# Performance work log

Hardware: AMD Instinct MI355X
Metric: run time of the kernel (lower is better)

## Reference

```python
import jax, jax.numpy as jnp
import numpy as np

N_TOK, TOKDIM = 2048, 1024
NHEADS, KDIM = 16, 64


def setup_inputs() -> dict:
    key = jax.random.key(0)
    kg, kk, kq = jax.random.split(key, 3)
    g = jax.random.normal(kg, (N_TOK, TOKDIM), dtype=jnp.float32)
    # params use normal(stddev=0.002) init, as in the flax module
    Wk = 0.002 * jax.random.normal(kk, (NHEADS, KDIM, TOKDIM), dtype=jnp.float32)
    Wq = 0.002 * jax.random.normal(kq, (NHEADS, KDIM, TOKDIM), dtype=jnp.float32)
    return {"g": g, "Wk": Wk, "Wq": Wq}


def reference(g, Wk, Wq):
    """manual_grad of the attention energy: returns d(energy)/dg, shape [n, d]."""
    H, Z, D = Wk.shape
    betas = jnp.full((H,), 1.0, dtype=g.dtype) / jnp.sqrt(jnp.asarray(Z, g.dtype))
    K = jnp.einsum('hzd,kd->khz', Wk, g)   # [n,h,z]
    Q = jnp.einsum('hzd,qd->qhz', Wq, g)   # [n,h,z]
    F1 = jnp.einsum('hzd,khz->khd', Wq, K)  # [n,h,d]
    F2 = jnp.einsum('hzd,qhz->qhd', Wk, Q)  # [n,h,d]
    A1 = jnp.einsum('h,khz,qhz->hqk', betas, K, Q)  # [h,q,k] scores
    A2 = jax.nn.softmax(A1, -1)
    T1 = -jnp.einsum('khd,hqk->qd', F1, A2)
    T2 = -jnp.einsum('qhd,hqk->kd', F2, A2)
    return T1 + T2
```

## Files before the change

### kernel.cpp

```cpp
#include <hip/hip_runtime.h>
#include <stdint.h>

#define NT 2048
#define TD 1024
#define NH 16
static constexpr float SCL = 0.18033688011112042f;

typedef __attribute__((ext_vector_type(8))) short bf16x8;
typedef __attribute__((ext_vector_type(4))) float f32x4;
typedef __attribute__((ext_vector_type(16))) float f32x16;
typedef __attribute__((address_space(3))) uint32_t lds_u32;
typedef __attribute__((address_space(1))) uint32_t glb_u32;

__device__ __forceinline__ float bf2f(unsigned short u){
  union { uint32_t u32; float f; } v; v.u32 = ((uint32_t)u) << 16; return v.f;
}
__device__ __forceinline__ unsigned short f2bf(float f){
  union { float f; uint32_t u; } v; v.f = f;
  uint32_t r = v.u + 0x7fffu + ((v.u >> 16) & 1u);
  return (unsigned short)(r >> 16);
}
__device__ __forceinline__ bf16x8 ld8(const unsigned short* base, int row, int kc){
  return *(const bf16x8*)((const char*)base + row*128 + ((kc ^ (row & 7)) << 4));
}
template<int N> __device__ __forceinline__ void wait_vm_lgkm0(){
  if constexpr (N == 0)      asm volatile("s_waitcnt vmcnt(0) lgkmcnt(0)" ::: "memory");
  else if constexpr (N == 4) asm volatile("s_waitcnt vmcnt(4) lgkmcnt(0)" ::: "memory");
  else if constexpr (N == 6) asm volatile("s_waitcnt vmcnt(6) lgkmcnt(0)" ::: "memory");
  __builtin_amdgcn_sched_barrier(0);
}

__global__ __launch_bounds__(256) void prep_kernel(
    const float* __restrict__ g, const float* __restrict__ Wk, const float* __restrict__ Wq,
    unsigned short* __restrict__ gbf, unsigned short* __restrict__ wkq,
    unsigned short* __restrict__ TWP)
{
  int b = blockIdx.x;
  if (b < 1024) {
    int base = b * 2048 + threadIdx.x;
    #pragma unroll
    for (int i = 0; i < 8; i++) { int idx = base + i * 256; gbf[idx] = f2bf(g[idx]); }
  } else if (b < 2048) {
    int base = (b - 1024) * 2048 + threadIdx.x;
    #pragma unroll
    for (int i = 0; i < 8; i++) {
      int idx = base + i * 256;
      float v = (idx < (1 << 20)) ? Wk[idx] : Wq[idx - (1 << 20)];
      wkq[idx] = f2bf(v);
    }
  } else {
    int t = b - 2048;
    int db = t & 31, jzg = t >> 5;
    int d0 = db * 32, j0 = jzg * 128;
    __shared__ unsigned short tile[128][33];
    int tid = threadIdx.x;
    const float* src = (j0 < 1024) ? Wq : Wk;
    int jb = (j0 < 1024) ? j0 : (j0 - 1024);
    #pragma unroll
    for (int i = 0; i < 16; i++) {
      int idx = i * 256 + tid, r = idx >> 5, c = idx & 31;
      tile[r][c] = f2bf(src[(size_t)(jb + r) * 1024 + d0 + c]);
    }
    __syncthreads();
    int jq = tid >> 6, l = tid & 63;
    #pragma unroll
    for (int f = 0; f < 2; f++) {
      int jzl = jq * 2 + f;
      unsigned short ob[8];
      #pragma unroll
      for (int e = 0; e < 8; e++)
        ob[e] = tile[jzl * 16 + 8 * (l >> 5) + e][l & 31];
      unsigned short* dst = TWP + ((size_t)(db * 128 + jzg * 8 + jzl) * 64 + l) * 8;
      *(ushort4*)dst       = *(ushort4*)&ob[0];
      *(ushort4*)(dst + 4) = *(ushort4*)&ob[4];
    }
  }
}

__global__ __launch_bounds__(256) void pack_pck(const unsigned short* __restrict__ CKQ,
                                                unsigned short* __restrict__ PCK)
{
  int tile = blockIdx.x;
  int cb = tile >> 6, rb = tile & 63;
  __shared__ unsigned short t[32][72];
  int tid = threadIdx.x;
  int r = tid >> 3, c0 = (tid & 7) * 8;
  const unsigned short* src = CKQ + (size_t)(rb * 32 + r) * 2048 + cb * 64 + c0;
  *(ushort4*)&t[r][c0]     = *(const ushort4*)src;
  *(ushort4*)&t[r][c0 + 4] = *(const ushort4*)(src + 4);
  __syncthreads();
  int kz = tid >> 6, l = tid & 63;
  int zl = kz * 16 + 8 * (l >> 5);
  ushort4 lo = *(ushort4*)&t[l & 31][zl];
  ushort4 hi4 = *(ushort4*)&t[l & 31][zl + 4];
  unsigned short* dst = PCK + ((size_t)(tile * 4 + kz) * 64 + l) * 8;
  *(ushort4*)dst       = lo;
  *(ushort4*)(dst + 4) = hi4;
}

template<bool DIVL>
__global__ __launch_bounds__(256) void pack_pbx(const unsigned short* __restrict__ CKQ,
                                                const float* __restrict__ L,
                                                unsigned short* __restrict__ PBX)
{
  int bid = blockIdx.x;
  int qb = bid & 63, hz = bid >> 6;
  int h = hz >> 1, zb = hz & 1;
  int colbase = (DIVL ? 1024 : 0) + h * 64 + zb * 32;
  __shared__ unsigned short tq[32][36];
  __shared__ float rcpL[32];
  int tid = threadIdx.x;
  int r = tid >> 3, c0 = (tid & 7) * 4;
  *(ushort4*)&tq[r][c0] =
      *(const ushort4*)(CKQ + (size_t)(qb * 32 + r) * 2048 + colbase + c0);
  if (DIVL && tid < 32) rcpL[tid] = 1.0f / L[(size_t)h * NT + qb * 32 + tid];
  __syncthreads();
  if (tid < 128) {
    int ks = tid >> 6, l = tid & 63;
    int zl = l & 31, hi = l >> 5;
    unsigned short ob[8];
    #pragma unroll
    for (int e = 0; e < 8; e++) {
      int ql = 16 * ks + 8 * (e >> 2) + 4 * hi + (e & 3);
      unsigned short v = tq[ql][zl];
      if (DIVL) v = f2bf(bf2f(v) * rcpL[ql]);
      ob[e] = v;
    }
    unsigned short* dst = PBX + ((size_t)(bid * 2 + ks) * 64 + l) * 8;
    *(ushort4*)dst       = *(ushort4*)&ob[0];
    *(ushort4*)(dst + 4) = *(ushort4*)&ob[4];
  }
}

template<int TM, int TN, int EPI, int WPE>
__global__ __launch_bounds__(256, WPE) void btg2_kernel(
    const unsigned short* __restrict__ A, int lda,
    const unsigned short* __restrict__ BT, int ldb,
    int Kdim, void* C0)
{
  constexpr int WM = TM / 2, WN = TN / 2, FM = WM / 16, FN = WN / 16;
  constexpr int AC = TM / 32, BC = TN / 32, LOADS = AC + BC;
  __shared__ __align__(16) unsigned short As[3][TM * 64];
  __shared__ __align__(16) unsigned short Bs[3][TN * 64];
  int tid = threadIdx.x, lane = tid & 63, wave = tid >> 6;
  int wr = wave >> 1, wc = wave & 1, lrow = lane & 15, g = lane >> 4;
  int bm = blockIdx.x * TM, bn = blockIdx.y * TN;

  auto stage = [&](unsigned short* bufA, unsigned short* bufB, int kk) {
    #pragma unroll
    for (int i = 0; i < AC; i++) {
      int c = i * 256 + tid, row = c >> 3, sl = ((c & 7) ^ (row & 7)) << 3;
      __builtin_amdgcn_global_load_lds((glb_u32*)(A + (size_t)(bm + row) * lda + kk + sl),
          (lds_u32*)((char*)bufA + i * 4096 + wave * 1024), 16, 0, 0);
    }
    #pragma unroll
    for (int i = 0; i < BC; i++) {
      int c = i * 256 + tid, row = c >> 3, sl = ((c & 7) ^ (row & 7)) << 3;
      __builtin_amdgcn_global_load_lds((glb_u32*)(BT + (size_t)(bn + row) * ldb + kk + sl),
          (lds_u32*)((char*)bufB + i * 4096 + wave * 1024), 16, 0, 0);
    }
  };

  f32x4 acc[FM][FN] = {};
  int nt = Kdim >> 6;
  stage(As[0], Bs[0], 0);
  stage(As[1], Bs[1], 64);
  wait_vm_lgkm0<LOADS>();
  __builtin_amdgcn_s_barrier();
  int bc = 0;
  for (int t = 0; t < nt; t++) {
    int bp = bc + 2; if (bp >= 3) bp -= 3;
    if (t + 2 < nt) stage(As[bp], Bs[bp], (t + 2) * 64);
    const unsigned short* Ac = As[bc];
    const unsigned short* Bc = Bs[bc];
    #pragma unroll
    for (int k2 = 0; k2 < 2; k2++) {
      bf16x8 a_[FM], b_[FN];
      #pragma unroll
      for (int m = 0; m < FM; m++) a_[m] = ld8(Ac, wr * WM + m * 16 + lrow, k2 * 4 + g);
      #pragma unroll
      for (int n = 0; n < FN; n++) b_[n] = ld8(Bc, wc * WN + n * 16 + lrow, k2 * 4 + g);
      #pragma unroll
      for (int m = 0; m < FM; m++)
        #pragma unroll
        for (int n = 0; n < FN; n++)
          acc[m][n] = __builtin_amdgcn_mfma_f32_16x16x32_bf16(a_[m], b_[n], acc[m][n], 0, 0, 0);
    }
    if (t + 2 < nt) wait_vm_lgkm0<LOADS>(); else wait_vm_lgkm0<0>();
    __builtin_amdgcn_s_barrier();
    bc = (bc == 2) ? 0 : bc + 1;
  }
  #pragma unroll
  for (int m = 0; m < FM; m++) {
    int rb = bm + wr * WM + m * 16 + 4 * g;
    #pragma unroll
    for (int n = 0; n < FN; n++) {
      int cc = bn + wc * WN + n * 16 + lrow;
      f32x4 v = acc[m][n];
      unsigned short* Cp = (unsigned short*)C0;
      #pragma unroll
      for (int j = 0; j < 4; j++) Cp[(size_t)(rb + j) * 2048 + cc] = f2bf(v[j]);
    }
  }
}

template<bool DIV>
__global__ __launch_bounds__(256, 2) void fused_kernel(
    const unsigned short* __restrict__ PCK,
    const unsigned short* __restrict__ PBX,
    unsigned short* __restrict__ PA,
    float* __restrict__ Lg)
{
  __shared__ __align__(16) float Red[2][64][68];
  __shared__ float L_lds[64];
  int tid = threadIdx.x, l = tid & 63, w = tid >> 6;
  int zr = l & 31, hi = l >> 5;
  int lin = blockIdx.x;
  int wgid = (lin & 7) * 64 + (lin >> 3);
  int h = wgid >> 5, pB = wgid & 31, p0 = pB * 64;
  int cbA = DIV ? h : 16 + h;
  int cbB = DIV ? 16 + h : h;
  const bf16x8* PCKf = (const bf16x8*)PCK;
  const bf16x8* PBXf = (const bf16x8*)PBX;

  bf16x8 bs[2][4];
  #pragma unroll
  for (int ps = 0; ps < 2; ps++)
    #pragma unroll
    for (int kz = 0; kz < 4; kz++)
      bs[ps][kz] = PCKf[((size_t)(cbB * 64 + pB * 2 + ps) * 4 + kz) * 64 + l];

  auto load = [&](bf16x8 (&a_)[4], bf16x8 (&pb_)[2][2], int rb){
    #pragma unroll
    for (int kz = 0; kz < 4; kz++)
      a_[kz] = PCKf[((size_t)(cbA * 64 + rb) * 4 + kz) * 64 + l];
    #pragma unroll
    for (int zb = 0; zb < 2; zb++)
      #pragma unroll
      for (int ks = 0; ks < 2; ks++)
        pb_[zb][ks] = PBXf[((size_t)((h * 2 + zb) * 64 + rb) * 2 + ks) * 64 + l];
  };

  f32x16 acc_pv[2][2] = {};
  float lsum[2] = {0.f, 0.f};
  bf16x8 a_c[4], pb_c[2][2];
  load(a_c, pb_c, w * 16);

  for (int t = 0; t < 16; t++) {
    bf16x8 a_n[4], pb_n[2][2];
    if (t + 1 < 16) load(a_n, pb_n, w * 16 + t + 1);
    f32x16 acc_s[2] = {};
    #pragma unroll
    for (int kz = 0; kz < 4; kz++) {
      acc_s[0] = __builtin_amdgcn_mfma_f32_32x32x16_bf16(a_c[kz], bs[0][kz], acc_s[0], 0, 0, 0);
      acc_s[1] = __builtin_amdgcn_mfma_f32_32x32x16_bf16(a_c[kz], bs[1][kz], acc_s[1], 0, 0, 0);
    }
    union { bf16x8 v; uint32_t u[4]; } pu[2][2];
    #pragma unroll
    for (int ps = 0; ps < 2; ps++) {
      float ev[16];
      #pragma unroll
      for (int r = 0; r < 16; r++) ev[r] = exp2f(acc_s[ps][r] * SCL);
      if (DIV) {
        #pragma unroll
        for (int r = 0; r < 16; r++) lsum[ps] += ev[r];
      }
      #pragma unroll
      for (int ks = 0; ks < 2; ks++)
        #pragma unroll
        for (int i = 0; i < 4; i++)
          asm("v_cvt_pk_bf16_f32 %0, %1, %2"
              : "=v"(pu[ps][ks].u[i]) : "v"(ev[8 * ks + 2 * i]), "v"(ev[8 * ks + 2 * i + 1]));
    }
    #pragma unroll
    for (int zb = 0; zb < 2; zb++)
      #pragma unroll
      for (int ks = 0; ks < 2; ks++) {
        acc_pv[0][zb] = __builtin_amdgcn_mfma_f32_32x32x16_bf16(pu[0][ks].v, pb_c[zb][ks], acc_pv[0][zb], 0, 0, 0);
        acc_pv[1][zb] = __builtin_amdgcn_mfma_f32_32x32x16_bf16(pu[1][ks].v, pb_c[zb][ks], acc_pv[1][zb], 0, 0, 0);
      }
    #pragma unroll
    for (int kz = 0; kz < 4; kz++) a_c[kz] = a_n[kz];
    #pragma unroll
    for (int zb = 0; zb < 2; zb++)
      #pragma unroll
      for (int ks = 0; ks < 2; ks++) pb_c[zb][ks] = pb_n[zb][ks];
  }

  if (w >= 2) {
    #pragma unroll
    for (int ps = 0; ps < 2; ps++)
      #pragma unroll
      for (int zb = 0; zb < 2; zb++) {
        int z = zb * 32 + zr;
        #pragma unroll
        for (int u = 0; u < 4; u++) {
          int p = ps * 32 + 8 * u + 4 * hi;
          f32x4 q;
          q[0] = acc_pv[ps][zb][4 * u];     q[1] = acc_pv[ps][zb][4 * u + 1];
          q[2] = acc_pv[ps][zb][4 * u + 2]; q[3] = acc_pv[ps][zb][4 * u + 3];
          *(f32x4*)&Red[w - 2][z][p] = q;
        }
      }
  }
  if (DIV && tid < 64) L_lds[tid] = 0.f;
  __syncthreads();
  if (w < 2) {
    #pragma unroll
    for (int ps = 0; ps < 2; ps++)
      #pragma unroll
      for (int zb = 0; zb < 2; zb++) {
        int z = zb * 32 + zr;
        #pragma unroll
        for (int u = 0; u < 4; u++) {
          int p = ps * 32 + 8 * u + 4 * hi;
          float* slot = &Red[w][z][p];
          f32x4 q = *(f32x4*)slot;
          q[0] += acc_pv[ps][zb][4 * u];     q[1] += acc_pv[ps][zb][4 * u + 1];
          q[2] += acc_pv[ps][zb][4 * u + 2]; q[3] += acc_pv[ps][zb][4 * u + 3];
          *(f32x4*)slot = q;
        }
      }
  }
  if (DIV) {
    #pragma unroll
    for (int ps = 0; ps < 2; ps++) {
      float s = lsum[ps];
      s += __shfl_xor(s, 32);
      if (hi == 0) atomicAdd(&L_lds[ps * 32 + zr], s);
    }
  }
  __syncthreads();
  if (DIV && tid < 64) Lg[(size_t)h * NT + p0 + tid] = L_lds[tid];
  int p = tid >> 2, z16 = (tid & 3) * 16;
  float inv = DIV ? 1.0f / L_lds[p] : 1.0f;
  int cbase = DIV ? h * 64 : TD + h * 64;
  int jz = (cbase + z16) >> 4;
  int tok = p0 + p, tb = tok >> 5, tl = tok & 31;
  unsigned short ob[16];
  #pragma unroll
  for (int i = 0; i < 16; i++) {
    int z = z16 + i;
    float x = Red[0][z][p] + Red[1][z][p];
    ob[i] = f2bf(x * inv);
  }
  unsigned short* dst = PA + (((size_t)jz * 64 + tb) * 64) * 8;
  *(ushort4*)(dst + tl * 8)            = *(ushort4*)&ob[0];
  *(ushort4*)(dst + tl * 8 + 4)        = *(ushort4*)&ob[4];
  *(ushort4*)(dst + (32 + tl) * 8)     = *(ushort4*)&ob[8];
  *(ushort4*)(dst + (32 + tl) * 8 + 4) = *(ushort4*)&ob[12];
}

__global__ __launch_bounds__(256, 2) void out_kernel(
    const unsigned short* __restrict__ PA,
    const unsigned short* __restrict__ TWP,
    float* __restrict__ out)
{
  __shared__ __align__(16) float Red[2][64][68];
  int tid = threadIdx.x, l = tid & 63, w = tid >> 6;
  int zr = l & 31, hi = l >> 5;
  int lin = blockIdx.x;
  int wgid = (lin & 7) * 64 + (lin >> 3);
  int tokb = wgid >> 4, db2 = wgid & 15;
  const bf16x8* PAf = (const bf16x8*)PA;
  const bf16x8* TWf = (const bf16x8*)TWP;

  f32x16 acc[2][2] = {};
  bf16x8 a_c[2], b_c[2];
  auto loadx = [&](bf16x8 (&a_)[2], bf16x8 (&b_)[2], int jz){
    #pragma unroll
    for (int th = 0; th < 2; th++)
      a_[th] = PAf[((size_t)jz * 64 + tokb * 2 + th) * 64 + l];
    #pragma unroll
    for (int dh = 0; dh < 2; dh++)
      b_[dh] = TWf[((size_t)(db2 * 2 + dh) * 128 + jz) * 64 + l];
  };
  loadx(a_c, b_c, w * 32);
  for (int it = 0; it < 32; it++) {
    bf16x8 a_n[2], b_n[2];
    if (it + 1 < 32) loadx(a_n, b_n, w * 32 + it + 1);
    #pragma unroll
    for (int th = 0; th < 2; th++)
      #pragma unroll
      for (int dh = 0; dh < 2; dh++)
        acc[th][dh] = __builtin_amdgcn_mfma_f32_32x32x16_bf16(a_c[th], b_c[dh], acc[th][dh], 0, 0, 0);
    #pragma unroll
    for (int i = 0; i < 2; i++) { a_c[i] = a_n[i]; b_c[i] = b_n[i]; }
  }
  if (w >= 2) {
    #pragma unroll
    for (int th = 0; th < 2; th++)
      #pragma unroll
      for (int dh = 0; dh < 2; dh++) {
        int d = dh * 32 + zr;
        #pragma unroll
        for (int u = 0; u < 4; u++) {
          int tk = th * 32 + 8 * u + 4 * hi;
          f32x4 q;
          q[0] = acc[th][dh][4 * u];     q[1] = acc[th][dh][4 * u + 1];
          q[2] = acc[th][dh][4 * u + 2]; q[3] = acc[th][dh][4 * u + 3];
          *(f32x4*)&Red[w - 2][d][tk] = q;
        }
      }
  }
  __syncthreads();
  if (w < 2) {
    #pragma unroll
    for (int th = 0; th < 2; th++)
      #pragma unroll
      for (int dh = 0; dh < 2; dh++) {
        int d = dh * 32 + zr;
        #pragma unroll
        for (int u = 0; u < 4; u++) {
          int tk = th * 32 + 8 * u + 4 * hi;
          float* slot = &Red[w][d][tk];
          f32x4 q = *(f32x4*)slot;
          q[0] += acc[th][dh][4 * u];     q[1] += acc[th][dh][4 * u + 1];
          q[2] += acc[th][dh][4 * u + 2]; q[3] += acc[th][dh][4 * u + 3];
          *(f32x4*)slot = q;
        }
      }
  }
  __syncthreads();
  int p = tid >> 2, d16 = (tid & 3) * 16;
  float* dst = out + (size_t)(tokb * 64 + p) * 1024 + db2 * 64 + d16;
  #pragma unroll
  for (int i4 = 0; i4 < 16; i4 += 4) {
    f32x4 r;
    #pragma unroll
    for (int j = 0; j < 4; j++)
      r[j] = -(Red[0][d16 + i4 + j][p] + Red[1][d16 + i4 + j][p]);
    *(f32x4*)(dst + i4) = r;
  }
}

extern "C" void kernel_launch(void* const* d_in, const int* in_sizes, int n_in,
                              void* d_out, int out_size, void* d_ws, size_t ws_size,
                              hipStream_t stream)
{
  (void)in_sizes; (void)n_in; (void)out_size; (void)ws_size;
  const float* g  = (const float*)d_in[0];
  const float* Wk = (const float*)d_in[1];
  const float* Wq = (const float*)d_in[2];

  char* ws = (char*)d_ws;
  size_t off = 0;
  auto alloc = [&](size_t b) -> char* {
    char* p = ws + off; off += (b + 255) & ~((size_t)255); return p;
  };
  unsigned short* gbf  = (unsigned short*)alloc((size_t)NT * TD * 2);
  unsigned short* wkq  = (unsigned short*)alloc((size_t)2 * TD * TD * 2);
  unsigned short* TWP  = (unsigned short*)alloc((size_t)TD * 2048 * 2);
  unsigned short* CKQ  = (unsigned short*)alloc((size_t)NT * 2048 * 2);
  unsigned short* PCK  = (unsigned short*)alloc((size_t)NT * 2048 * 2);
  unsigned short* PBT  = (unsigned short*)alloc((size_t)TD * NT * 2);
  unsigned short* QSTP = (unsigned short*)alloc((size_t)TD * NT * 2);
  unsigned short* PA   = (unsigned short*)alloc((size_t)NT * 2048 * 2);
  float*          Lbuf = (float*)alloc((size_t)NH * NT * 4);

  prep_kernel<<<dim3(2560), dim3(256), 0, stream>>>(g, Wk, Wq, gbf, wkq, TWP);

  btg2_kernel<128, 64, 0, 2><<<dim3(16, 32), dim3(256), 0, stream>>>(
      gbf, TD, wkq, TD, TD, (void*)CKQ);

  pack_pck<<<dim3(2048), dim3(256), 0, stream>>>(CKQ, PCK);
  pack_pbx<false><<<dim3(2048), dim3(256), 0, stream>>>(CKQ, nullptr, PBT);

  fused_kernel<true><<<dim3(512), dim3(256), 0, stream>>>(PCK, PBT, PA, Lbuf);

  pack_pbx<true><<<dim3(2048), dim3(256), 0, stream>>>(CKQ, Lbuf, QSTP);

  fused_kernel<false><<<dim3(512), dim3(256), 0, stream>>>(PCK, QSTP, PA, nullptr);

  out_kernel<<<dim3(512), dim3(256), 0, stream>>>(PA, TWP, (float*)d_out);
}
```

Measured before the change: 107.1 us.

## Pre-pack operands into MFMA fragment layout and fuse K/Q projection with PCK packing

The prep kernel now writes g and the Wk/Wq weights directly in a per-lane MFMA fragment layout. A new kq_kernel computes the K/Q projection with 32x32x16 MFMAs, using register double-buffered loads straight from global memory and an LDS reduction across the split-K waves. It writes both the row-major CKQ and the packed PCK layout, so the separate pack_pck launch and its CKQ reread are gone. In exchange it drops the LDS-staged, swizzled, triple-buffered GEMM and relies on fragment-coalesced global loads plus a split-K reduction through shared memory.

```diff
diff --git a/kernel.cpp b/kernel.cpp
--- a/kernel.cpp
+++ b/kernel.cpp
@@ -9,8 +9,6 @@
 typedef __attribute__((ext_vector_type(8))) short bf16x8;
 typedef __attribute__((ext_vector_type(4))) float f32x4;
 typedef __attribute__((ext_vector_type(16))) float f32x16;
-typedef __attribute__((address_space(3))) uint32_t lds_u32;
-typedef __attribute__((address_space(1))) uint32_t glb_u32;
 
 __device__ __forceinline__ float bf2f(unsigned short u){
   union { uint32_t u32; float f; } v; v.u32 = ((uint32_t)u) << 16; return v.f;
@@ -20,40 +18,43 @@
   uint32_t r = v.u + 0x7fffu + ((v.u >> 16) & 1u);
   return (unsigned short)(r >> 16);
 }
-__device__ __forceinline__ bf16x8 ld8(const unsigned short* base, int row, int kc){
-  return *(const bf16x8*)((const char*)base + row*128 + ((kc ^ (row & 7)) << 4));
-}
-template<int N> __device__ __forceinline__ void wait_vm_lgkm0(){
-  if constexpr (N == 0)      asm volatile("s_waitcnt vmcnt(0) lgkmcnt(0)" ::: "memory");
-  else if constexpr (N == 4) asm volatile("s_waitcnt vmcnt(4) lgkmcnt(0)" ::: "memory");
-  else if constexpr (N == 6) asm volatile("s_waitcnt vmcnt(6) lgkmcnt(0)" ::: "memory");
-  __builtin_amdgcn_sched_barrier(0);
-}
 
 __global__ __launch_bounds__(256) void prep_kernel(
     const float* __restrict__ g, const float* __restrict__ Wk, const float* __restrict__ Wq,
-    unsigned short* __restrict__ gbf, unsigned short* __restrict__ wkq,
+    unsigned short* __restrict__ PG, unsigned short* __restrict__ PW,
     unsigned short* __restrict__ TWP)
 {
   int b = blockIdx.x;
-  if (b < 1024) {
-    int base = b * 2048 + threadIdx.x;
-    #pragma unroll
-    for (int i = 0; i < 8; i++) { int idx = base + i * 256; gbf[idx] = f2bf(g[idx]); }
-  } else if (b < 2048) {
-    int base = (b - 1024) * 2048 + threadIdx.x;
-    #pragma unroll
-    for (int i = 0; i < 8; i++) {
-      int idx = base + i * 256;
-      float v = (idx < (1 << 20)) ? Wk[idx] : Wq[idx - (1 << 20)];
-      wkq[idx] = f2bf(v);
-    }
+  int tid = threadIdx.x;
+  if (b < 2048) {
+    bool isW = (b >= 1024);
+    int bb = isW ? b - 1024 : b;
+    int dg = bb & 15, rb2 = bb >> 4;
+    __shared__ float tile[32][65];
+    const float* src;
+    int rbase;
+    if (!isW) { src = g; rbase = rb2 * 32; }
+    else if (rb2 < 32) { src = Wk; rbase = rb2 * 32; }
+    else { src = Wq; rbase = rb2 * 32 - 1024; }
+    int r = tid >> 3, c0 = (tid & 7) * 8;
+    const float* s = src + (size_t)(rbase + r) * 1024 + dg * 64 + c0;
+    *(f32x4*)&tile[r][c0]     = *(const f32x4*)s;
+    *(f32x4*)&tile[r][c0 + 4] = *(const f32x4*)(s + 4);
+    __syncthreads();
+    int dzl = tid >> 6, l = tid & 63;
+    int dz = dg * 4 + dzl;
+    unsigned short ob[8];
+    #pragma unroll
+    for (int e = 0; e < 8; e++)
+      ob[e] = f2bf(tile[l & 31][dzl * 16 + 8 * (l >> 5) + e]);
+    unsigned short* dst = (isW ? PW : PG) + ((size_t)(rb2 * 64 + dz) * 64 + l) * 8;
+    *(ushort4*)dst       = *(ushort4*)&ob[0];
+    *(ushort4*)(dst + 4) = *(ushort4*)&ob[4];
   } else {
     int t = b - 2048;
     int db = t & 31, jzg = t >> 5;
     int d0 = db * 32, j0 = jzg * 128;
     __shared__ unsigned short tile[128][33];
-    int tid = threadIdx.x;
     const float* src = (j0 < 1024) ? Wq : Wk;
     int jb = (j0 < 1024) ? j0 : (j0 - 1024);
     #pragma unroll
@@ -77,25 +78,95 @@
   }
 }
 
-__global__ __launch_bounds__(256) void pack_pck(const unsigned short* __restrict__ CKQ,
-                                                unsigned short* __restrict__ PCK)
-{
-  int tile = blockIdx.x;
-  int cb = tile >> 6, rb = tile & 63;
-  __shared__ unsigned short t[32][72];
-  int tid = threadIdx.x;
-  int r = tid >> 3, c0 = (tid & 7) * 8;
-  const unsigned short* src = CKQ + (size_t)(rb * 32 + r) * 2048 + cb * 64 + c0;
-  *(ushort4*)&t[r][c0]     = *(const ushort4*)src;
-  *(ushort4*)&t[r][c0 + 4] = *(const ushort4*)(src + 4);
-  __syncthreads();
-  int kz = tid >> 6, l = tid & 63;
-  int zl = kz * 16 + 8 * (l >> 5);
-  ushort4 lo = *(ushort4*)&t[l & 31][zl];
-  ushort4 hi4 = *(ushort4*)&t[l & 31][zl + 4];
-  unsigned short* dst = PCK + ((size_t)(tile * 4 + kz) * 64 + l) * 8;
-  *(ushort4*)dst       = lo;
-  *(ushort4*)(dst + 4) = hi4;
+__global__ __launch_bounds__(256, 2) void kq_kernel(
+    const unsigned short* __restrict__ PG,
+    const unsigned short* __restrict__ PW,
+    unsigned short* __restrict__ CKQ,
+    unsigned short* __restrict__ PCK)
+{
+  __shared__ __align__(16) float Red[2][64][68];
+  int tid = threadIdx.x, l = tid & 63, w = tid >> 6;
+  int zr = l & 31, hi = l >> 5;
+  int lin = blockIdx.x;
+  int wgid = (lin & 7) * 128 + (lin >> 3);
+  int tokb = wgid >> 5, cblk = wgid & 31;
+  const bf16x8* PGf = (const bf16x8*)PG;
+  const bf16x8* PWf = (const bf16x8*)PW;
+
+  f32x16 acc[2][2] = {};
+  bf16x8 a_c[2], b_c[2];
+  auto loadx = [&](bf16x8 (&a_)[2], bf16x8 (&b_)[2], int dz){
+    #pragma unroll
+    for (int th = 0; th < 2; th++)
+      a_[th] = PGf[((size_t)(tokb * 2 + th) * 64 + dz) * 64 + l];
+    #pragma unroll
+    for (int ch = 0; ch < 2; ch++)
+      b_[ch] = PWf[((size_t)(cblk * 2 + ch) * 64 + dz) * 64 + l];
+  };
+  loadx(a_c, b_c, w * 16);
+  for (int it = 0; it < 16; it++) {
+    bf16x8 a_n[2], b_n[2];
+    if (it + 1 < 16) loadx(a_n, b_n, w * 16 + it + 1);
+    #pragma unroll
+    for (int th = 0; th < 2; th++)
+      #pragma unroll
+      for (int ch = 0; ch < 2; ch++)
+        acc[th][ch] = __builtin_amdgcn_mfma_f32_32x32x16_bf16(a_c[th], b_c[ch], acc[th][ch], 0, 0, 0);
+    #pragma unroll
+    for (int i = 0; i < 2; i++) { a_c[i] = a_n[i]; b_c[i] = b_n[i]; }
+  }
+  if (w >= 2) {
+    #pragma unroll
+    for (int th = 0; th < 2; th++)
+      #pragma unroll
+      for (int ch = 0; ch < 2; ch++) {
+        int c = ch * 32 + zr;
+        #pragma unroll
+        for (int u = 0; u < 4; u++) {
+          int tk = th * 32 + 8 * u + 4 * hi;
+          f32x4 q;
+          q[0] = acc[th][ch][4 * u];     q[1] = acc[th][ch][4 * u + 1];
+          q[2] = acc[th][ch][4 * u + 2]; q[3] = acc[th][ch][4 * u + 3];
+          *(f32x4*)&Red[w - 2][c][tk] = q;
+        }
+      }
+  }
+  __syncthreads();
+  if (w < 2) {
+    #pragma unroll
+    for (int th = 0; th < 2; th++)
+      #pragma unroll
+      for (int ch = 0; ch < 2; ch++) {
+        int c = ch * 32 + zr;
+        #pragma unroll
+        for (int u = 0; u < 4; u++) {
+          int tk = th * 32 + 8 * u + 4 * hi;
+          float* slot = &Red[w][c][tk];
+          f32x4 q = *(f32x4*)slot;
+          q[0] += acc[th][ch][4 * u];     q[1] += acc[th][ch][4 * u + 1];
+          q[2] += acc[th][ch][4 * u + 2]; q[3] += acc[th][ch][4 * u + 3];
+          *(f32x4*)slot = q;
+        }
+      }
+  }
+  __syncthreads();
+  int p = tid >> 2, c16 = (tid & 3) * 16;
+  int tok = tokb * 64 + p;
+  unsigned short ob[16];
+  #pragma unroll
+  for (int i = 0; i < 16; i++)
+    ob[i] = f2bf(Red[0][c16 + i][p] + Red[1][c16 + i][p]);
+  unsigned short* dst = CKQ + (size_t)tok * 2048 + cblk * 64 + c16;
+  *(ushort4*)dst        = *(ushort4*)&ob[0];
+  *(ushort4*)(dst + 4)  = *(ushort4*)&ob[4];
+  *(ushort4*)(dst + 8)  = *(ushort4*)&ob[8];
+  *(ushort4*)(dst + 12) = *(ushort4*)&ob[12];
+  int rb = tok >> 5, tl = tok & 31, kz = tid & 3;
+  unsigned short* dstp = PCK + (((size_t)(cblk * 64 + rb) * 4 + kz) * 64) * 8;
+  *(ushort4*)(dstp + tl * 8)            = *(ushort4*)&ob[0];
+  *(ushort4*)(dstp + tl * 8 + 4)        = *(ushort4*)&ob[4];
+  *(ushort4*)(dstp + (32 + tl) * 8)     = *(ushort4*)&ob[8];
+  *(ushort4*)(dstp + (32 + tl) * 8 + 4) = *(ushort4*)&ob[12];
 }
 
 template<bool DIVL>
@@ -129,78 +200,6 @@
     unsigned short* dst = PBX + ((size_t)(bid * 2 + ks) * 64 + l) * 8;
     *(ushort4*)dst       = *(ushort4*)&ob[0];
     *(ushort4*)(dst + 4) = *(ushort4*)&ob[4];
-  }
-}
-
-template<int TM, int TN, int EPI, int WPE>
-__global__ __launch_bounds__(256, WPE) void btg2_kernel(
-    const unsigned short* __restrict__ A, int lda,
-    const unsigned short* __restrict__ BT, int ldb,
-    int Kdim, void* C0)
-{
-  constexpr int WM = TM / 2, WN = TN / 2, FM = WM / 16, FN = WN / 16;
-  constexpr int AC = TM / 32, BC = TN / 32, LOADS = AC + BC;
-  __shared__ __align__(16) unsigned short As[3][TM * 64];
-  __shared__ __align__(16) unsigned short Bs[3][TN * 64];
-  int tid = threadIdx.x, lane = tid & 63, wave = tid >> 6;
-  int wr = wave >> 1, wc = wave & 1, lrow = lane & 15, g = lane >> 4;
-  int bm = blockIdx.x * TM, bn = blockIdx.y * TN;
-
-  auto stage = [&](unsigned short* bufA, unsigned short* bufB, int kk) {
-    #pragma unroll
-    for (int i = 0; i < AC; i++) {
-      int c = i * 256 + tid, row = c >> 3, sl = ((c & 7) ^ (row & 7)) << 3;
-      __builtin_amdgcn_global_load_lds((glb_u32*)(A + (size_t)(bm + row) * lda + kk + sl),
-          (lds_u32*)((char*)bufA + i * 4096 + wave * 1024), 16, 0, 0);
-    }
-    #pragma unroll
-    for (int i = 0; i < BC; i++) {
-      int c = i * 256 + tid, row = c >> 3, sl = ((c & 7) ^ (row & 7)) << 3;
-      __builtin_amdgcn_global_load_lds((glb_u32*)(BT + (size_t)(bn + row) * ldb + kk + sl),
-          (lds_u32*)((char*)bufB + i * 4096 + wave * 1024), 16, 0, 0);
-    }
-  };
-
-  f32x4 acc[FM][FN] = {};
-  int nt = Kdim >> 6;
-  stage(As[0], Bs[0], 0);
-  stage(As[1], Bs[1], 64);
-  wait_vm_lgkm0<LOADS>();
-  __builtin_amdgcn_s_barrier();
-  int bc = 0;
-  for (int t = 0; t < nt; t++) {
-    int bp = bc + 2; if (bp >= 3) bp -= 3;
-    if (t + 2 < nt) stage(As[bp], Bs[bp], (t + 2) * 64);
-    const unsigned short* Ac = As[bc];
-    const unsigned short* Bc = Bs[bc];
-    #pragma unroll
-    for (int k2 = 0; k2 < 2; k2++) {
-      bf16x8 a_[FM], b_[FN];
-      #pragma unroll
-      for (int m = 0; m < FM; m++) a_[m] = ld8(Ac, wr * WM + m * 16 + lrow, k2 * 4 + g);
-      #pragma unroll
-      for (int n = 0; n < FN; n++) b_[n] = ld8(Bc, wc * WN + n * 16 + lrow, k2 * 4 + g);
-      #pragma unroll
-      for (int m = 0; m < FM; m++)
-        #pragma unroll
-        for (int n = 0; n < FN; n++)
-          acc[m][n] = __builtin_amdgcn_mfma_f32_16x16x32_bf16(a_[m], b_[n], acc[m][n], 0, 0, 0);
-    }
-    if (t + 2 < nt) wait_vm_lgkm0<LOADS>(); else wait_vm_lgkm0<0>();
-    __builtin_amdgcn_s_barrier();
-    bc = (bc == 2) ? 0 : bc + 1;
-  }
-  #pragma unroll
-  for (int m = 0; m < FM; m++) {
-    int rb = bm + wr * WM + m * 16 + 4 * g;
-    #pragma unroll
-    for (int n = 0; n < FN; n++) {
-      int cc = bn + wc * WN + n * 16 + lrow;
-      f32x4 v = acc[m][n];
-      unsigned short* Cp = (unsigned short*)C0;
-      #pragma unroll
-      for (int j = 0; j < 4; j++) Cp[(size_t)(rb + j) * 2048 + cc] = f2bf(v[j]);
-    }
   }
 }
 
@@ -448,8 +447,8 @@
   auto alloc = [&](size_t b) -> char* {
     char* p = ws + off; off += (b + 255) & ~((size_t)255); return p;
   };
-  unsigned short* gbf  = (unsigned short*)alloc((size_t)NT * TD * 2);
-  unsigned short* wkq  = (unsigned short*)alloc((size_t)2 * TD * TD * 2);
+  unsigned short* PG   = (unsigned short*)alloc((size_t)NT * TD * 2);
+  unsigned short* PW   = (unsigned short*)alloc((size_t)2048 * TD * 2);
   unsigned short* TWP  = (unsigned short*)alloc((size_t)TD * 2048 * 2);
   unsigned short* CKQ  = (unsigned short*)alloc((size_t)NT * 2048 * 2);
   unsigned short* PCK  = (unsigned short*)alloc((size_t)NT * 2048 * 2);
@@ -458,12 +457,10 @@
   unsigned short* PA   = (unsigned short*)alloc((size_t)NT * 2048 * 2);
   float*          Lbuf = (float*)alloc((size_t)NH * NT * 4);
 
-  prep_kernel<<<dim3(2560), dim3(256), 0, stream>>>(g, Wk, Wq, gbf, wkq, TWP);
-
-  btg2_kernel<128, 64, 0, 2><<<dim3(16, 32), dim3(256), 0, stream>>>(
-      gbf, TD, wkq, TD, TD, (void*)CKQ);
-
-  pack_pck<<<dim3(2048), dim3(256), 0, stream>>>(CKQ, PCK);
+  prep_kernel<<<dim3(2560), dim3(256), 0, stream>>>(g, Wk, Wq, PG, PW, TWP);
+
+  kq_kernel<<<dim3(1024), dim3(256), 0, stream>>>(PG, PW, CKQ, PCK);
+
   pack_pbx<false><<<dim3(2048), dim3(256), 0, stream>>>(CKQ, nullptr, PBT);
 
   fused_kernel<true><<<dim3(512), dim3(256), 0, stream>>>(PCK, PBT, PA, Lbuf);
```

Result: faster. 104.6 us (-2.3%).
